# Optimization experiments

Measured on AMD Instinct MI355X. Metric: run time of the kernel, lower is better.

Reference implementation:

```python
import jax, jax.numpy as jnp
import numpy as np
from jax import lax

BATCH = 8192
PATCH = 2
STRIDE = 2
OUT_CH = 4
NUM_PATCHES = ((28 - PATCH) // STRIDE + 1) ** 2  # 196
THRESHOLD = 0.8
EPS = 1e-12


def setup_inputs() -> dict:
    key = jax.random.key(0)
    k1, k2, k3, k4, k5 = jax.random.split(key, 5)
    x = jax.random.normal(k1, (BATCH, 1, 28, 28), dtype=jnp.float32)
    conv_w = jax.random.normal(k2, (OUT_CH, 1, PATCH, PATCH), dtype=jnp.float32) * 0.5
    conv_b = jax.random.normal(k3, (OUT_CH,), dtype=jnp.float32) * 0.1
    feat_dim = OUT_CH * NUM_PATCHES + NUM_PATCHES  # 784 + 196 = 980
    lin_w = jax.random.normal(k4, (10, feat_dim), dtype=jnp.float32) * 0.02
    lin_b = jax.random.normal(k5, (10,), dtype=jnp.float32) * 0.01
    return {"x": x, "conv_w": conv_w, "conv_b": conv_b, "lin_w": lin_w, "lin_b": lin_b}


def reference(x, conv_w, conv_b, lin_w, lin_b):
    # conv patch embed: (B,1,28,28) -> (B,C,14,14)
    f = lax.conv_general_dilated(
        x, conv_w, window_strides=(STRIDE, STRIDE), padding="VALID",
        dimension_numbers=("NCHW", "OIHW", "NCHW"))
    f = f + conv_b[None, :, None, None]
    B = f.shape[0]
    flat = f.reshape(B, -1)  # (B, C*P) channel-major, matches torch .view
    # replicate feat.view(num_patches, -1): rows of length C from the flat vector
    pf = flat.reshape(B, NUM_PATCHES, -1)  # (B, P, C)
    nrm = pf / (jnp.linalg.norm(pf, axis=-1, keepdims=True) + EPS)
    # squared cosine similarity = state fidelity, all pairs at once
    fid = jnp.einsum("bpc,bqc->bpq", nrm, nrm) ** 2  # (B, P, P)
    w = (fid >= THRESHOLD).astype(flat.dtype)
    w = w * (1.0 - jnp.eye(NUM_PATCHES, dtype=flat.dtype))  # no self-edges
    deg = jnp.sum(w, axis=-1)  # weighted degree per node, (B, P)
    feats = jnp.concatenate([flat, deg], axis=1)  # (B, 980)
    logits = feats @ lin_w.T + lin_b
    return jax.nn.log_softmax(logits, axis=-1)
```

## Files before the change

kernel.cpp:

```cpp
#include <hip/hip_runtime.h>
#include <math.h>


#define NP 196
#define FEAT 980
#define COS_TH 0.894427190999915878f

typedef float v2f __attribute__((ext_vector_type(2)));
typedef float v4f __attribute__((ext_vector_type(4)));

__global__ __launch_bounds__(256, 6) void quanv_kernel(
    const float* __restrict__ x,
    const float* __restrict__ conv_w,
    const float* __restrict__ conv_b,
    const float* __restrict__ lin_w,
    const float* __restrict__ lin_b,
    float* __restrict__ out)
{
    __shared__ __align__(16) float s_x[784];
    __shared__ __align__(16) float s_n[4][256];
    __shared__ __align__(16) float s_feats[FEAT];

    unsigned* s_cnt   = (unsigned*)s_x;
    float*    s_part  = s_x + 256;
    float*    s_logits= s_x + 512;

    const int b = blockIdx.x;
    const int t = threadIdx.x;
    const int w = t >> 6, l = t & 63;

    if (t < NP) {
        ((float4*)s_x)[t] = ((const float4*)(x + (size_t)b * 784))[t];
    }
    __syncthreads();

    if (t < NP) {
        int h = t / 14, ww = t - 14 * (t / 14);
        const float* r0 = s_x + (2 * h) * 28 + 2 * ww;
        float x00 = r0[0], x01 = r0[1], x10 = r0[28], x11 = r0[29];
        #pragma unroll
        for (int c = 0; c < 4; ++c) {
            float f = conv_b[c]
                    + conv_w[c * 4 + 0] * x00 + conv_w[c * 4 + 1] * x01
                    + conv_w[c * 4 + 2] * x10 + conv_w[c * 4 + 3] * x11;
            s_feats[c * NP + t] = f;
        }
    }
    __syncthreads();

    if (t < NP) {
        float4 v = ((const float4*)s_feats)[t];
        float n = sqrtf(v.x * v.x + v.y * v.y + v.z * v.z + v.w * v.w);
        float inv = 1.0f / (n + 1e-12f);
        s_n[0][t] = v.x * inv; s_n[1][t] = v.y * inv;
        s_n[2][t] = v.z * inv; s_n[3][t] = v.w * inv;
    } else {
        s_n[0][t] = 0.f; s_n[1][t] = 0.f; s_n[2][t] = 0.f; s_n[3][t] = 0.f;
    }
    __syncthreads();

    {
        v2f mx[3], my[3], mz[3], mw[3];
        #pragma unroll
        for (int r = 0; r < 3; ++r) {
            int row = l + 64 * r;
            float px = s_n[0][row], py = s_n[1][row], pz = s_n[2][row], pw = s_n[3][row];
            mx[r] = (v2f){px, px};
            my[r] = (v2f){py, py};
            mz[r] = (v2f){pz, pz};
            mw[r] = (v2f){pw, pw};
        }
        #pragma unroll
        for (int r = 0; r < 3; ++r)
            asm("" : "+v"(mx[r]), "+v"(my[r]), "+v"(mz[r]), "+v"(mw[r]));

        unsigned cnt[3] = {0u, 0u, 0u};
        const float* qb = &s_n[0][52 * w];
        #pragma unroll
        for (int j = 0; j < 13; ++j) {
            v4f qx = *(const v4f*)(qb + 4 * j);
            v4f qy = *(const v4f*)(qb + 256 + 4 * j);
            v4f qz = *(const v4f*)(qb + 512 + 4 * j);
            v4f qw = *(const v4f*)(qb + 768 + 4 * j);
            v2f qx0 = __builtin_shufflevector(qx, qx, 0, 1);
            v2f qx1 = __builtin_shufflevector(qx, qx, 2, 3);
            v2f qy0 = __builtin_shufflevector(qy, qy, 0, 1);
            v2f qy1 = __builtin_shufflevector(qy, qy, 2, 3);
            v2f qz0 = __builtin_shufflevector(qz, qz, 0, 1);
            v2f qz1 = __builtin_shufflevector(qz, qz, 2, 3);
            v2f qw0 = __builtin_shufflevector(qw, qw, 0, 1);
            v2f qw1 = __builtin_shufflevector(qw, qw, 2, 3);
            #pragma unroll
            for (int r = 0; r < 3; ++r) {
                v2f d0, d1;
                asm("v_pk_mul_f32 %0, %1, %2"     : "=v"(d0) : "v"(qx0), "v"(mx[r]));
                asm("v_pk_mul_f32 %0, %1, %2"     : "=v"(d1) : "v"(qx1), "v"(mx[r]));
                asm("v_pk_fma_f32 %0, %1, %2, %0" : "+v"(d0) : "v"(qy0), "v"(my[r]));
                asm("v_pk_fma_f32 %0, %1, %2, %0" : "+v"(d1) : "v"(qy1), "v"(my[r]));
                asm("v_pk_fma_f32 %0, %1, %2, %0" : "+v"(d0) : "v"(qz0), "v"(mz[r]));
                asm("v_pk_fma_f32 %0, %1, %2, %0" : "+v"(d1) : "v"(qz1), "v"(mz[r]));
                asm("v_pk_fma_f32 %0, %1, %2, %0" : "+v"(d0) : "v"(qw0), "v"(mw[r]));
                asm("v_pk_fma_f32 %0, %1, %2, %0" : "+v"(d1) : "v"(qw1), "v"(mw[r]));
                cnt[r] += (fabsf(d0.x) >= COS_TH);
                cnt[r] += (fabsf(d0.y) >= COS_TH);
                cnt[r] += (fabsf(d1.x) >= COS_TH);
                cnt[r] += (fabsf(d1.y) >= COS_TH);
            }
        }
        s_cnt[t] = cnt[0] | (cnt[1] << 8) | (cnt[2] << 16);
    }

    {
        int row = 192 + w;
        float px = s_n[0][row], py = s_n[1][row], pz = s_n[2][row], pw = s_n[3][row];
        unsigned total = 0u;
        #pragma unroll
        for (int j = 0; j < 4; ++j) {
            int q = 64 * j + l;
            float d = px * s_n[0][q];
            d = fmaf(py, s_n[1][q], d);
            d = fmaf(pz, s_n[2][q], d);
            d = fmaf(pw, s_n[3][q], d);
            unsigned long long m = __ballot(fabsf(d) >= COS_TH);
            total += (unsigned)__popcll(m);
        }
        if (l == 0) s_feats[784 + row] = (float)(total - 1u);
    }
    __syncthreads();

    if (t < 192) {
        int c = t >> 6, ll = t & 63;
        unsigned s = ((s_cnt[ll]       >> (8 * c)) & 255u)
                   + ((s_cnt[64 + ll]  >> (8 * c)) & 255u)
                   + ((s_cnt[128 + ll] >> (8 * c)) & 255u)
                   + ((s_cnt[192 + ll] >> (8 * c)) & 255u);
        s_feats[784 + t] = (float)(s - 1u);
    }
    __syncthreads();

    if (t < 250) {
        int k = t / 25, c = t - 25 * (t / 25);
        const float4* wrow = (const float4*)(lin_w + k * FEAT);
        const float4* frow = (const float4*)s_feats;
        float acc = 0.0f;
        for (int i = c; i < 245; i += 25) {
            float4 f = frow[i];
            float4 wv = wrow[i];
            acc = fmaf(f.x, wv.x, acc);
            acc = fmaf(f.y, wv.y, acc);
            acc = fmaf(f.z, wv.z, acc);
            acc = fmaf(f.w, wv.w, acc);
        }
        s_part[t] = acc;
    }
    __syncthreads();

    if (t < 10) {
        float s = lin_b[t];
        #pragma unroll
        for (int i = 0; i < 25; ++i) s += s_part[t * 25 + i];
        s_logits[t] = s;
    }
    __syncthreads();

    if (t < 10) {
        float m = -INFINITY;
        #pragma unroll
        for (int j = 0; j < 10; ++j) m = fmaxf(m, s_logits[j]);
        float s = 0.0f;
        #pragma unroll
        for (int j = 0; j < 10; ++j) s += expf(s_logits[j] - m);
        out[(size_t)b * 10 + t] = s_logits[t] - m - logf(s);
    }
}

extern "C" void kernel_launch(void* const* d_in, const int* in_sizes, int n_in,
                              void* d_out, int out_size, void* d_ws, size_t ws_size,
                              hipStream_t stream) {
    const float* x      = (const float*)d_in[0];
    const float* conv_w = (const float*)d_in[1];
    const float* conv_b = (const float*)d_in[2];
    const float* lin_w  = (const float*)d_in[3];
    const float* lin_b  = (const float*)d_in[4];
    float* out = (float*)d_out;
    quanv_kernel<<<dim3(8192), dim3(256), 0, stream>>>(x, conv_w, conv_b, lin_w, lin_b, out);
}
```

Measured before the change: 123.6 us.

## Process two images per block to amortize lin_w loads and barriers

Each block now handles two batch images, with their shared-memory buffers doubled, and the grid is halved to 4096 blocks. The linear layer loads each lin_w element once and applies it to both images, and the block's barriers and setup are shared across two images. The cost is roughly double the shared memory per block (about 19 KB), which may limit how many blocks fit per CU. The pairwise similarity phase now runs the two images back to back, so each block has a longer serial critical path.

```diff
diff --git a/kernel.cpp b/kernel.cpp
--- a/kernel.cpp
+++ b/kernel.cpp
@@ -17,54 +17,61 @@
     const float* __restrict__ lin_b,
     float* __restrict__ out)
 {
-    __shared__ __align__(16) float s_x[784];
-    __shared__ __align__(16) float s_n[4][256];
-    __shared__ __align__(16) float s_feats[FEAT];
-
-    unsigned* s_cnt   = (unsigned*)s_x;
-    float*    s_part  = s_x + 256;
-    float*    s_logits= s_x + 512;
+    __shared__ __align__(16) float s_x[2][784];
+    __shared__ __align__(16) float s_n[2][4][256];
+    __shared__ __align__(16) float s_feats[2][FEAT];
 
     const int b = blockIdx.x;
     const int t = threadIdx.x;
     const int w = t >> 6, l = t & 63;
 
     if (t < NP) {
-        ((float4*)s_x)[t] = ((const float4*)(x + (size_t)b * 784))[t];
+        ((float4*)s_x[0])[t] = ((const float4*)(x + (size_t)(2 * b)     * 784))[t];
+        ((float4*)s_x[1])[t] = ((const float4*)(x + (size_t)(2 * b + 1) * 784))[t];
     }
     __syncthreads();
 
     if (t < NP) {
         int h = t / 14, ww = t - 14 * (t / 14);
-        const float* r0 = s_x + (2 * h) * 28 + 2 * ww;
-        float x00 = r0[0], x01 = r0[1], x10 = r0[28], x11 = r0[29];
-        #pragma unroll
-        for (int c = 0; c < 4; ++c) {
-            float f = conv_b[c]
-                    + conv_w[c * 4 + 0] * x00 + conv_w[c * 4 + 1] * x01
-                    + conv_w[c * 4 + 2] * x10 + conv_w[c * 4 + 3] * x11;
-            s_feats[c * NP + t] = f;
-        }
-    }
-    __syncthreads();
-
-    if (t < NP) {
-        float4 v = ((const float4*)s_feats)[t];
-        float n = sqrtf(v.x * v.x + v.y * v.y + v.z * v.z + v.w * v.w);
-        float inv = 1.0f / (n + 1e-12f);
-        s_n[0][t] = v.x * inv; s_n[1][t] = v.y * inv;
-        s_n[2][t] = v.z * inv; s_n[3][t] = v.w * inv;
-    } else {
-        s_n[0][t] = 0.f; s_n[1][t] = 0.f; s_n[2][t] = 0.f; s_n[3][t] = 0.f;
-    }
-    __syncthreads();
-
-    {
+        #pragma unroll
+        for (int img = 0; img < 2; ++img) {
+            const float* r0 = s_x[img] + (2 * h) * 28 + 2 * ww;
+            float x00 = r0[0], x01 = r0[1], x10 = r0[28], x11 = r0[29];
+            #pragma unroll
+            for (int c = 0; c < 4; ++c) {
+                float f = conv_b[c]
+                        + conv_w[c * 4 + 0] * x00 + conv_w[c * 4 + 1] * x01
+                        + conv_w[c * 4 + 2] * x10 + conv_w[c * 4 + 3] * x11;
+                s_feats[img][c * NP + t] = f;
+            }
+        }
+    }
+    __syncthreads();
+
+    #pragma unroll
+    for (int img = 0; img < 2; ++img) {
+        if (t < NP) {
+            float4 v = ((const float4*)s_feats[img])[t];
+            float n = sqrtf(v.x * v.x + v.y * v.y + v.z * v.z + v.w * v.w);
+            float inv = 1.0f / (n + 1e-12f);
+            s_n[img][0][t] = v.x * inv; s_n[img][1][t] = v.y * inv;
+            s_n[img][2][t] = v.z * inv; s_n[img][3][t] = v.w * inv;
+        } else {
+            s_n[img][0][t] = 0.f; s_n[img][1][t] = 0.f;
+            s_n[img][2][t] = 0.f; s_n[img][3][t] = 0.f;
+        }
+    }
+    __syncthreads();
+
+    #pragma unroll
+    for (int img = 0; img < 2; ++img) {
+        unsigned* s_cnt = (unsigned*)s_x[img];
         v2f mx[3], my[3], mz[3], mw[3];
         #pragma unroll
         for (int r = 0; r < 3; ++r) {
             int row = l + 64 * r;
-            float px = s_n[0][row], py = s_n[1][row], pz = s_n[2][row], pw = s_n[3][row];
+            float px = s_n[img][0][row], py = s_n[img][1][row];
+            float pz = s_n[img][2][row], pw = s_n[img][3][row];
             mx[r] = (v2f){px, px};
             my[r] = (v2f){py, py};
             mz[r] = (v2f){pz, pz};
@@ -75,7 +82,7 @@
             asm("" : "+v"(mx[r]), "+v"(my[r]), "+v"(mz[r]), "+v"(mw[r]));
 
         unsigned cnt[3] = {0u, 0u, 0u};
-        const float* qb = &s_n[0][52 * w];
+        const float* qb = &s_n[img][0][52 * w];
         #pragma unroll
         for (int j = 0; j < 13; ++j) {
             v4f qx = *(const v4f*)(qb + 4 * j);
@@ -108,69 +115,79 @@
             }
         }
         s_cnt[t] = cnt[0] | (cnt[1] << 8) | (cnt[2] << 16);
-    }
-
-    {
+
         int row = 192 + w;
-        float px = s_n[0][row], py = s_n[1][row], pz = s_n[2][row], pw = s_n[3][row];
+        float px = s_n[img][0][row], py = s_n[img][1][row];
+        float pz = s_n[img][2][row], pw = s_n[img][3][row];
         unsigned total = 0u;
         #pragma unroll
         for (int j = 0; j < 4; ++j) {
             int q = 64 * j + l;
-            float d = px * s_n[0][q];
-            d = fmaf(py, s_n[1][q], d);
-            d = fmaf(pz, s_n[2][q], d);
-            d = fmaf(pw, s_n[3][q], d);
+            float d = px * s_n[img][0][q];
+            d = fmaf(py, s_n[img][1][q], d);
+            d = fmaf(pz, s_n[img][2][q], d);
+            d = fmaf(pw, s_n[img][3][q], d);
             unsigned long long m = __ballot(fabsf(d) >= COS_TH);
             total += (unsigned)__popcll(m);
         }
-        if (l == 0) s_feats[784 + row] = (float)(total - 1u);
+        if (l == 0) s_feats[img][784 + row] = (float)(total - 1u);
     }
     __syncthreads();
 
     if (t < 192) {
         int c = t >> 6, ll = t & 63;
-        unsigned s = ((s_cnt[ll]       >> (8 * c)) & 255u)
-                   + ((s_cnt[64 + ll]  >> (8 * c)) & 255u)
-                   + ((s_cnt[128 + ll] >> (8 * c)) & 255u)
-                   + ((s_cnt[192 + ll] >> (8 * c)) & 255u);
-        s_feats[784 + t] = (float)(s - 1u);
+        #pragma unroll
+        for (int img = 0; img < 2; ++img) {
+            const unsigned* s_cnt = (const unsigned*)s_x[img];
+            unsigned s = ((s_cnt[ll]       >> (8 * c)) & 255u)
+                       + ((s_cnt[64 + ll]  >> (8 * c)) & 255u)
+                       + ((s_cnt[128 + ll] >> (8 * c)) & 255u)
+                       + ((s_cnt[192 + ll] >> (8 * c)) & 255u);
+            s_feats[img][784 + t] = (float)(s - 1u);
+        }
     }
     __syncthreads();
 
     if (t < 250) {
         int k = t / 25, c = t - 25 * (t / 25);
         const float4* wrow = (const float4*)(lin_w + k * FEAT);
-        const float4* frow = (const float4*)s_feats;
-        float acc = 0.0f;
+        const float4* f0p = (const float4*)s_feats[0];
+        const float4* f1p = (const float4*)s_feats[1];
+        float a0 = 0.0f, a1 = 0.0f;
         for (int i = c; i < 245; i += 25) {
-            float4 f = frow[i];
             float4 wv = wrow[i];
-            acc = fmaf(f.x, wv.x, acc);
-            acc = fmaf(f.y, wv.y, acc);
-            acc = fmaf(f.z, wv.z, acc);
-            acc = fmaf(f.w, wv.w, acc);
-        }
-        s_part[t] = acc;
-    }
-    __syncthreads();
-
-    if (t < 10) {
-        float s = lin_b[t];
-        #pragma unroll
-        for (int i = 0; i < 25; ++i) s += s_part[t * 25 + i];
-        s_logits[t] = s;
-    }
-    __syncthreads();
-
-    if (t < 10) {
+            float4 f0 = f0p[i];
+            float4 f1 = f1p[i];
+            a0 = fmaf(f0.x, wv.x, a0); a1 = fmaf(f1.x, wv.x, a1);
+            a0 = fmaf(f0.y, wv.y, a0); a1 = fmaf(f1.y, wv.y, a1);
+            a0 = fmaf(f0.z, wv.z, a0); a1 = fmaf(f1.z, wv.z, a1);
+            a0 = fmaf(f0.w, wv.w, a0); a1 = fmaf(f1.w, wv.w, a1);
+        }
+        (s_x[0] + 256)[t] = a0;
+        (s_x[1] + 256)[t] = a1;
+    }
+    __syncthreads();
+
+    if (t < 20) {
+        int img = t / 10, k = t - 10 * (t / 10);
+        const float* part = s_x[img] + 256;
+        float s = lin_b[k];
+        #pragma unroll
+        for (int i = 0; i < 25; ++i) s += part[k * 25 + i];
+        (s_x[img] + 512)[k] = s;
+    }
+    __syncthreads();
+
+    if (t < 20) {
+        int img = t / 10, k = t - 10 * (t / 10);
+        const float* lg = s_x[img] + 512;
         float m = -INFINITY;
         #pragma unroll
-        for (int j = 0; j < 10; ++j) m = fmaxf(m, s_logits[j]);
+        for (int j = 0; j < 10; ++j) m = fmaxf(m, lg[j]);
         float s = 0.0f;
         #pragma unroll
-        for (int j = 0; j < 10; ++j) s += expf(s_logits[j] - m);
-        out[(size_t)b * 10 + t] = s_logits[t] - m - logf(s);
+        for (int j = 0; j < 10; ++j) s += expf(lg[j] - m);
+        out[(size_t)(2 * b + img) * 10 + k] = lg[k] - m - logf(s);
     }
 }
 
@@ -183,5 +200,5 @@
     const float* lin_w  = (const float*)d_in[3];
     const float* lin_b  = (const float*)d_in[4];
     float* out = (float*)d_out;
-    quanv_kernel<<<dim3(8192), dim3(256), 0, stream>>>(x, conv_w, conv_b, lin_w, lin_b, out);
+    quanv_kernel<<<dim3(4096), dim3(256), 0, stream>>>(x, conv_w, conv_b, lin_w, lin_b, out);
 }
```

Result: faster. 120.5 us (-2.5%).
